# Performance work log

Measured on AMD Instinct MI355X. Metric: run time of the kernel, lower is better.

Reference implementation:

```python
import jax, jax.numpy as jnp
import numpy as np
from jax import lax

NQ = 4      # num_qubits
DEPTH = 2
DIM = 2 ** NQ  # 16

def _maxpool2(x):
    # MaxPool2d(kernel_size=2, stride=1), NCHW
    return lax.reduce_window(x, -jnp.inf, lax.max, (1, 1, 2, 2), (1, 1, 1, 1), 'VALID')

def _conv(x, w, b, stride, pad):
    y = lax.conv_general_dilated(x, w, (stride, stride), [(pad, pad), (pad, pad)],
                                 dimension_numbers=('NCHW', 'OIHW', 'NCHW'))
    return y + b[None, :, None, None]

def _apply_1q(state, gate, q):
    # state: (B, 16) complex64; gate: (2,2) shared or (B,2,2) per-sample. wire 0 = MSB.
    B = state.shape[0]
    s = state.reshape(B, 2 ** q, 2, 2 ** (NQ - 1 - q))
    sub = 'ij,bljr->blir' if gate.ndim == 2 else 'bij,bljr->blir'
    return jnp.einsum(sub, gate, s).reshape(B, DIM)

def _quantum_head(angles, weights):
    # Batched statevector simulation of: RX(angles[i]) encoding, then DEPTH x
    # [RY(w) on every wire, CZ chain], then <Z_0>, <Z_1>.
    B = angles.shape[0]
    state = jnp.zeros((B, DIM), jnp.complex64).at[:, 0].set(1.0)
    for q in range(NQ):  # RX encoding (per-sample angles)
        t = angles[:, q] * 0.5
        c = jnp.cos(t).astype(jnp.complex64)
        s = (-1j) * jnp.sin(t).astype(jnp.complex64)
        gate = jnp.stack([jnp.stack([c, s], -1), jnp.stack([s, c], -1)], -2)  # (B,2,2)
        state = _apply_1q(state, gate, q)
    idxs = jnp.arange(DIM)
    w_idx = 0
    for _ in range(DEPTH):
        for q in range(NQ):  # RY(weights) shared across batch
            t = weights[w_idx] * 0.5
            w_idx += 1
            c, s = jnp.cos(t), jnp.sin(t)
            gate = jnp.stack([jnp.stack([c, -s]), jnp.stack([s, c])]).astype(jnp.complex64)
            state = _apply_1q(state, gate, q)
        for q in range(NQ - 1):  # CZ(q, q+1): -1 phase where both bits set
            both = ((idxs >> (NQ - 1 - q)) & 1) & ((idxs >> (NQ - 2 - q)) & 1)
            phase = jnp.where(both == 1, -1.0, 1.0).astype(jnp.complex64)
            state = state * phase[None, :]
    probs = state.real ** 2 + state.imag ** 2  # (B,16) float32
    logits = []
    for q in range(2):  # expval PauliZ on wires 0,1
        sign = 1.0 - 2.0 * ((idxs >> (NQ - 1 - q)) & 1).astype(jnp.float32)
        logits.append(probs @ sign)
    return jnp.stack(logits, -1)  # (B,2)


def setup_inputs() -> dict:
    key = jax.random.key(0)
    ks = jax.random.split(key, 12)
    x = jax.random.normal(ks[0], (256, 3, 250, 250), jnp.float32)
    w1 = jax.random.normal(ks[1], (6, 3, 5, 5), jnp.float32) * 0.05
    b1 = jnp.zeros((6,), jnp.float32)
    w2 = jax.random.normal(ks[2], (15, 6, 3, 3), jnp.float32) * 0.05
    b2 = jnp.zeros((15,), jnp.float32)
    fc1_w = jax.random.normal(ks[3], (120, 55815), jnp.float32) * 0.004
    fc1_b = jnp.zeros((120,), jnp.float32)
    fc2_w = jax.random.normal(ks[4], (84, 120), jnp.float32) * 0.09
    fc2_b = jnp.zeros((84,), jnp.float32)
    fc3_w = jax.random.normal(ks[5], (4, 84), jnp.float32) * 0.1
    fc3_b = jnp.zeros((4,), jnp.float32)
    qweights = jax.random.normal(ks[6], (NQ * DEPTH,), jnp.float32)
    return {'x': x, 'w1': w1, 'b1': b1, 'w2': w2, 'b2': b2,
            'fc1_w': fc1_w, 'fc1_b': fc1_b, 'fc2_w': fc2_w, 'fc2_b': fc2_b,
            'fc3_w': fc3_w, 'fc3_b': fc3_b, 'qweights': qweights}


def reference(x, w1, b1, w2, b2, fc1_w, fc1_b, fc2_w, fc2_b, fc3_w, fc3_b, qweights):
    # Dropout layers act as identity (eval mode).
    h = jax.nn.relu(_conv(x, w1, b1, stride=2, pad=1))   # (B,6,124,124)
    h = _maxpool2(h)                                      # (B,6,123,123)
    h = jax.nn.relu(_conv(h, w2, b2, stride=2, pad=1))   # (B,15,62,62)
    h = _maxpool2(h)                                      # (B,15,61,61)
    h = h.reshape(h.shape[0], -1)                         # (B,55815)
    h = jax.nn.relu(h @ fc1_w.T + fc1_b)
    h = jax.nn.relu(h @ fc2_w.T + fc2_b)
    angles = h @ fc3_w.T + fc3_b                          # (B,4)
    logits = _quantum_head(angles, qweights)              # (B,2)
    return jax.nn.softmax(logits, axis=-1)
```

## Files before the change

kernel.cpp:

```cpp
#include <hip/hip_runtime.h>
#include <hip/hip_bf16.h>
#include <hip/hip_fp16.h>
#include <math.h>

#define B 256
#define FC1_K   55815
#define FC1_N   120
#define FC2_N   84
#define KP        57344
#define FC1_SPLIT 256
#define FC1_KC    (KP / FC1_SPLIT)

typedef __attribute__((ext_vector_type(8))) short bf16x8;
typedef __attribute__((ext_vector_type(4))) float f32x4;
typedef _Float16 half2_t __attribute__((ext_vector_type(2)));

static __device__ __forceinline__ unsigned short bf16_bits(float f) {
    __hip_bfloat16 h = __float2bfloat16(f);
    return *(unsigned short*)&h;
}
static __device__ __forceinline__ unsigned short f16_bits(float f) {
    __half h = __float2half(f);
    return *(unsigned short*)&h;
}
static __device__ __forceinline__ half2_t h2_from_u32(unsigned int u) {
    return __builtin_bit_cast(half2_t, u);
}

#define ASYNC_CP(g, l) __builtin_amdgcn_global_load_lds( \
    (const __attribute__((address_space(1))) void*)(g),  \
    (__attribute__((address_space(3))) void*)(l), 4, 0, 0)

__global__ __launch_bounds__(256) void conv1_fused_kernel(
    const float* __restrict__ x, const float* __restrict__ w1,
    const float* __restrict__ b1, const float* __restrict__ fc1_w,
    unsigned short* __restrict__ pool1, float* __restrict__ zeros,
    unsigned short* __restrict__ wb) {
    if (blockIdx.x >= 18) {
        int wid = (blockIdx.x - 18) * 256 + blockIdx.y;
        int kb = wid >> 7, n = wid & 127;
        int k0 = kb * 2048 + threadIdx.x * 8;
        bf16x8 v8;
        #pragma unroll
        for (int i = 0; i < 8; ++i) v8[i] = 0;
        if (n < FC1_N) {
            const float* src = fc1_w + (size_t)n * FC1_K + k0;
            if (k0 + 8 <= FC1_K) {
                #pragma unroll
                for (int i = 0; i < 8; ++i) v8[i] = (short)bf16_bits(src[i]);
            } else {
                #pragma unroll
                for (int i = 0; i < 8; ++i)
                    if (k0 + i < FC1_K) v8[i] = (short)bf16_bits(src[i]);
            }
        }
        *(bf16x8*)(wb + (size_t)n * KP + k0) = v8;
        return;
    }

    __shared__ __align__(16) float in_t[19 * 256 + 8];
    __shared__ __align__(16) unsigned short out_t[6 * 8 * 132];

    const int tid = threadIdx.x;
    const int wave = tid >> 6, lane = tid & 63;
    const int PB = 7 * blockIdx.x;
    const int b  = blockIdx.y;
    const int cg = tid & 31, rr = tid >> 5;
    const int iyb = 2 * PB - 1;

    if (tid < 64) zeros[tid] = 0.f;

    float acc[4][6];
    #pragma unroll
    for (int j = 0; j < 4; ++j)
        #pragma unroll
        for (int o = 0; o < 6; ++o) acc[j][o] = b1[o];

    for (int c = 0; c < 3; ++c) {
        __syncthreads();
        const float* xp = x + (size_t)(b * 3 + c) * 62500;
        #pragma unroll
        for (int i = 0; i < 19; ++i) {
            int chunk = wave * 19 + i;
            int f = chunk * 64 + lane;
            int row = f >> 8, m = f & 255;
            int iy = iyb + row, col = m - 1;
            const float* g = ((unsigned)iy < 250u && (unsigned)col < 250u)
                             ? (xp + iy * 250 + col) : zeros;
            ASYNC_CP(g, &in_t[chunk * 64]);
        }
        __syncthreads();
        #pragma unroll
        for (int ky = 0; ky < 5; ++ky) {
            const float* rp = &in_t[(2 * rr + ky) * 256 + 8 * cg];
            float f[12];
            float4 v0 = *(const float4*)rp;
            float4 v1 = *(const float4*)(rp + 4);
            float4 v2 = *(const float4*)(rp + 8);
            f[0]=v0.x; f[1]=v0.y; f[2]=v0.z; f[3]=v0.w;
            f[4]=v1.x; f[5]=v1.y; f[6]=v1.z; f[7]=v1.w;
            f[8]=v2.x; f[9]=v2.y; f[10]=v2.z; f[11]=v2.w;
            #pragma unroll
            for (int kx = 0; kx < 5; ++kx) {
                #pragma unroll
                for (int j = 0; j < 4; ++j) {
                    float xv = f[2 * j + kx];
                    #pragma unroll
                    for (int o = 0; o < 6; ++o)
                        acc[j][o] += xv * w1[(o * 3 + c) * 25 + ky * 5 + kx];
                }
            }
        }
    }
    #pragma unroll
    for (int o = 0; o < 6; ++o) {
        unsigned short h0 = f16_bits(fmaxf(acc[0][o], 0.f));
        unsigned short h1 = f16_bits(fmaxf(acc[1][o], 0.f));
        unsigned short h2 = f16_bits(fmaxf(acc[2][o], 0.f));
        unsigned short h3 = f16_bits(fmaxf(acc[3][o], 0.f));
        uint2 pk;
        pk.x = (unsigned)h0 | ((unsigned)h1 << 16);
        pk.y = (unsigned)h2 | ((unsigned)h3 << 16);
        *(uint2*)&out_t[(o * 8 + rr) * 132 + 4 * cg] = pk;
    }
    __syncthreads();
    for (int it = tid; it < 6 * 7 * 32; it += 256) {
        int g = it & 31, rem = it >> 5;
        int pyl = rem % 7, oc = rem / 7;
        int py = PB + pyl;
        if (py >= 123) continue;
        const unsigned short* q0 = &out_t[(oc * 8 + pyl) * 132 + 4 * g];
        const unsigned short* q1 = q0 + 132;
        uint2 ua = *(const uint2*)q0;
        uint2 ub = *(const uint2*)q1;
        unsigned short va[5] = {(unsigned short)(ua.x & 0xffff), (unsigned short)(ua.x >> 16),
                                (unsigned short)(ua.y & 0xffff), (unsigned short)(ua.y >> 16), q0[4]};
        unsigned short vb[5] = {(unsigned short)(ub.x & 0xffff), (unsigned short)(ub.x >> 16),
                                (unsigned short)(ub.y & 0xffff), (unsigned short)(ub.y >> 16), q1[4]};
        unsigned short* dst = pool1 + ((size_t)(b * 6 + oc) * 123 + py) * 128;
        #pragma unroll
        for (int j = 0; j < 4; ++j) {
            int px = 4 * g + j;
            if (px >= 127) continue;
            unsigned short m = 0;
            if (px <= 122) {
                unsigned short m0 = va[j] > va[j+1] ? va[j] : va[j+1];
                unsigned short m1 = vb[j] > vb[j+1] ? vb[j] : vb[j+1];
                m = m0 > m1 ? m0 : m1;
            }
            dst[1 + px] = m;
        }
        if (g == 0) dst[0] = 0;
    }
}

__global__ __launch_bounds__(128) void conv2_pool2_kernel(
    const unsigned short* __restrict__ pool1, const float* __restrict__ w2,
    const float* __restrict__ b2, unsigned short* __restrict__ A) {
    __shared__ __align__(16) unsigned int in2[17 * 64 + 8];
    __shared__ __align__(16) unsigned int wlds[540];
    __shared__ __align__(16) unsigned short out2[15 * 8 * 68];

    const int tid = threadIdx.x;
    const int wave = tid >> 6, lane = tid & 63;
    const int PB = 7 * blockIdx.x;
    const int b  = blockIdx.y;
    const int cg = tid & 15, rr = tid >> 4;
    const int iyb = 2 * PB - 1;

    for (int f = tid; f < 540; f += 128) {
        int pr = f & 1, g = f >> 1;
        int o = g % 15, r = g / 15, ky = r % 3, c = r / 3;
        const float* wsrc = w2 + (o * 6 + c) * 9 + ky * 3;
        unsigned int pk;
        if (pr == 0) pk = (unsigned)f16_bits(wsrc[0]) | ((unsigned)f16_bits(wsrc[1]) << 16);
        else         pk = (unsigned)f16_bits(wsrc[2]);
        wlds[((c * 3 + ky) * 15 + o) * 2 + pr] = pk;
    }
    if (tid < 8) in2[17 * 64 + tid] = 0;

    float acc[4][15];
    #pragma unroll
    for (int j = 0; j < 4; ++j)
        #pragma unroll
        for (int o = 0; o < 15; ++o) acc[j][o] = b2[o];

    const unsigned int* p1u = (const unsigned int*)pool1;
    for (int c = 0; c < 6; ++c) {
        __syncthreads();
        const unsigned int* pp = p1u + (size_t)(b * 6 + c) * (123 * 64);
        #pragma unroll
        for (int i = 0; i < 9; ++i) {
            int chunk = wave * 9 + i;
            if (chunk < 17) {
                int iy = iyb + chunk;
                if ((unsigned)iy < 123u) {
                    ASYNC_CP(pp + iy * 64 + lane, &in2[chunk * 64]);
                } else {
                    in2[chunk * 64 + lane] = 0;
                }
            }
        }
        __syncthreads();
        #pragma unroll
        for (int ky = 0; ky < 3; ++ky) {
            const unsigned int* rp = &in2[(2 * rr + ky) * 64 + 4 * cg];
            half2_t dd[5];
            {
                uint4 u4 = *(const uint4*)rp;
                unsigned int u5 = rp[4];
                dd[0] = h2_from_u32(u4.x); dd[1] = h2_from_u32(u4.y);
                dd[2] = h2_from_u32(u4.z); dd[3] = h2_from_u32(u4.w);
                dd[4] = h2_from_u32(u5);
            }
            const unsigned int* wrow = &wlds[(c * 3 + ky) * 30];
            unsigned int wv[30];
            #pragma unroll
            for (int i = 0; i < 30; ++i) wv[i] = wrow[i];
            #pragma unroll
            for (int j = 0; j < 4; ++j) {
                #pragma unroll
                for (int o = 0; o < 15; ++o) {
                    acc[j][o] = __builtin_amdgcn_fdot2(dd[j],     h2_from_u32(wv[o * 2]),
                                                       acc[j][o], false);
                    acc[j][o] = __builtin_amdgcn_fdot2(dd[j + 1], h2_from_u32(wv[o * 2 + 1]),
                                                       acc[j][o], false);
                }
            }
        }
    }
    #pragma unroll
    for (int o = 0; o < 15; ++o) {
        unsigned short h0 = bf16_bits(fmaxf(acc[0][o], 0.f));
        unsigned short h1 = bf16_bits(fmaxf(acc[1][o], 0.f));
        unsigned short h2 = bf16_bits(fmaxf(acc[2][o], 0.f));
        unsigned short h3 = bf16_bits(fmaxf(acc[3][o], 0.f));
        uint2 pk;
        pk.x = (unsigned)h0 | ((unsigned)h1 << 16);
        pk.y = (unsigned)h2 | ((unsigned)h3 << 16);
        *(uint2*)&out2[(o * 8 + rr) * 68 + 4 * cg] = pk;
    }
    __syncthreads();
    for (int it = tid; it < 15 * 7 * 16; it += 128) {
        int g = it & 15, rem = it >> 4;
        int pyl = rem % 7, oc = rem / 7;
        int py = PB + pyl;
        if (py >= 61) continue;
        const unsigned short* q0 = &out2[(oc * 8 + pyl) * 68 + 4 * g];
        const unsigned short* q1 = q0 + 68;
        uint2 ua = *(const uint2*)q0;
        uint2 ub = *(const uint2*)q1;
        unsigned short va[5] = {(unsigned short)(ua.x & 0xffff), (unsigned short)(ua.x >> 16),
                                (unsigned short)(ua.y & 0xffff), (unsigned short)(ua.y >> 16), q0[4]};
        unsigned short vb[5] = {(unsigned short)(ub.x & 0xffff), (unsigned short)(ub.x >> 16),
                                (unsigned short)(ub.y & 0xffff), (unsigned short)(ub.y >> 16), q1[4]};
        #pragma unroll
        for (int j = 0; j < 4; ++j) {
            int px = 4 * g + j;
            if (px < 61) {
                unsigned short m0 = va[j] > va[j+1] ? va[j] : va[j+1];
                unsigned short m1 = vb[j] > vb[j+1] ? vb[j] : vb[j+1];
                unsigned short m = m0 > m1 ? m0 : m1;
                A[(size_t)b * KP + (oc * 61 + py) * 61 + px] = m;
            }
        }
    }
}

__global__ __launch_bounds__(256) void fc1_mfma_kernel(
    const __hip_bfloat16* __restrict__ A, const __hip_bfloat16* __restrict__ W,
    float* __restrict__ partial) {
    const int wave = threadIdx.x >> 6, lane = threadIdx.x & 63;
    const int mrow = lane & 15, quad = lane >> 4;
    const int m0 = blockIdx.x * 128 + wave * 32;
    const int k0 = blockIdx.y * FC1_KC;

    f32x4 acc[2][8];
    #pragma unroll
    for (int i = 0; i < 2; ++i)
        #pragma unroll
        for (int j = 0; j < 8; ++j) acc[i][j] = (f32x4){0.f, 0.f, 0.f, 0.f};

    const short* Ap = (const short*)A;
    const short* Wp = (const short*)W;
    for (int ks = 0; ks < FC1_KC; ks += 32) {
        const int kk = k0 + ks + quad * 8;
        const bf16x8 a0 = *(const bf16x8*)(Ap + (size_t)(m0 + mrow) * KP + kk);
        const bf16x8 a1 = *(const bf16x8*)(Ap + (size_t)(m0 + 16 + mrow) * KP + kk);
        #pragma unroll
        for (int nt = 0; nt < 8; ++nt) {
            const bf16x8 bb = *(const bf16x8*)(Wp + (size_t)(nt * 16 + mrow) * KP + kk);
            acc[0][nt] = __builtin_amdgcn_mfma_f32_16x16x32_bf16(a0, bb, acc[0][nt], 0, 0, 0);
            acc[1][nt] = __builtin_amdgcn_mfma_f32_16x16x32_bf16(a1, bb, acc[1][nt], 0, 0, 0);
        }
    }
    float* po = partial + (size_t)blockIdx.y * (256 * 128);
    #pragma unroll
    for (int mt = 0; mt < 2; ++mt)
        #pragma unroll
        for (int nt = 0; nt < 8; ++nt)
            #pragma unroll
            for (int r = 0; r < 4; ++r)
                po[(m0 + mt * 16 + quad * 4 + r) * 128 + nt * 16 + mrow] = acc[mt][nt][r];
}

__global__ __launch_bounds__(512) void tail_kernel(
    const float* __restrict__ partial, const float* __restrict__ fc1_b,
    const float* __restrict__ fc2_w, const float* __restrict__ fc2_b,
    const float* __restrict__ fc3_w, const float* __restrict__ fc3_b,
    const float* __restrict__ qw, float* __restrict__ out) {
    __shared__ float h1p[4][FC1_N];
    __shared__ float h1[FC1_N];
    __shared__ float h2[FC2_N];
    __shared__ float ang[4];
    int b = blockIdx.x;
    int t = threadIdx.x;
    int grp = t >> 7, tt = t & 127;

    if (tt < FC1_N) {
        const float* p = partial + b * 128 + tt;
        float sum = 0.f;
        #pragma unroll 8
        for (int s = grp * 64; s < grp * 64 + 64; ++s) sum += p[(size_t)s * (256 * 128)];
        h1p[grp][tt] = sum;
    }
    __syncthreads();
    if (t < FC1_N)
        h1[t] = fmaxf(h1p[0][t] + h1p[1][t] + h1p[2][t] + h1p[3][t] + fc1_b[t], 0.f);
    __syncthreads();
    if (t < FC2_N) {
        float acc = fc2_b[t];
        const float* w = fc2_w + t * FC1_N;
        for (int k = 0; k < FC1_N; ++k) acc += h1[k] * w[k];
        h2[t] = fmaxf(acc, 0.f);
    }
    __syncthreads();
    if (t < 4) {
        float acc = fc3_b[t];
        const float* w = fc3_w + t * FC2_N;
        for (int k = 0; k < FC2_N; ++k) acc += h2[k] * w[k];
        ang[t] = acc;
    }
    __syncthreads();
    if (t < 16) {
        const int lane = t;
        float sr = (lane == 0) ? 1.f : 0.f, si = 0.f;
        #pragma unroll
        for (int q = 0; q < 4; ++q) {
            float th = ang[q] * 0.5f;
            float c = __cosf(th), s = __sinf(th);
            int mask = 8 >> q;
            float pr = __shfl_xor(sr, mask, 16);
            float pi = __shfl_xor(si, mask, 16);
            float nr = c * sr + s * pi;
            float ni = c * si - s * pr;
            sr = nr; si = ni;
        }
        int widx = 0;
        #pragma unroll
        for (int d = 0; d < 2; ++d) {
            #pragma unroll
            for (int q = 0; q < 4; ++q) {
                float th = qw[widx++] * 0.5f;
                float c = __cosf(th), s = __sinf(th);
                int mask = 8 >> q;
                float pr = __shfl_xor(sr, mask, 16);
                float pi = __shfl_xor(si, mask, 16);
                float sg = (lane & mask) ? s : -s;
                sr = c * sr + sg * pr;
                si = c * si + sg * pi;
            }
            #pragma unroll
            for (int q = 0; q < 3; ++q) {
                int m1 = 8 >> q, m2 = 4 >> q;
                if ((lane & m1) && (lane & m2)) { sr = -sr; si = -si; }
            }
        }
        float p = sr * sr + si * si;
        float v0 = (lane & 8) ? -p : p;
        float v1 = (lane & 4) ? -p : p;
        #pragma unroll
        for (int off = 8; off >= 1; off >>= 1) {
            v0 += __shfl_xor(v0, off, 16);
            v1 += __shfl_xor(v1, off, 16);
        }
        if (lane == 0) {
            float m = fmaxf(v0, v1);
            float e0 = expf(v0 - m), e1 = expf(v1 - m);
            float inv = 1.f / (e0 + e1);
            out[b * 2 + 0] = e0 * inv;
            out[b * 2 + 1] = e1 * inv;
        }
    }
}

extern "C" void kernel_launch(void* const* d_in, const int* in_sizes, int n_in,
                              void* d_out, int out_size, void* d_ws, size_t ws_size,
                              hipStream_t stream) {
    const float* x     = (const float*)d_in[0];
    const float* w1    = (const float*)d_in[1];
    const float* b1    = (const float*)d_in[2];
    const float* w2    = (const float*)d_in[3];
    const float* b2    = (const float*)d_in[4];
    const float* fc1_w = (const float*)d_in[5];
    const float* fc1_b = (const float*)d_in[6];
    const float* fc2_w = (const float*)d_in[7];
    const float* fc2_b = (const float*)d_in[8];
    const float* fc3_w = (const float*)d_in[9];
    const float* fc3_b = (const float*)d_in[10];
    const float* qw    = (const float*)d_in[11];
    float* out = (float*)d_out;

    char* ws = (char*)d_ws;
    const size_t O_POOL1  = 0;
    const size_t O_A      = O_POOL1 + 48365568;
    const size_t O_W      = O_A + 29360128;
    const size_t O_PART   = O_W + 14680064;
    const size_t O_ZERO   = O_PART + 33554432;
    unsigned short* pool1   = (unsigned short*)(ws + O_POOL1);
    __hip_bfloat16* A_bf16  = (__hip_bfloat16*)(ws + O_A);
    __hip_bfloat16* W_bf16  = (__hip_bfloat16*)(ws + O_W);
    float*          partial = (float*)(ws + O_PART);
    float*          zeros   = (float*)(ws + O_ZERO);

    conv1_fused_kernel<<<dim3(32, B), 256, 0, stream>>>(
        x, w1, b1, fc1_w, pool1, zeros, (unsigned short*)W_bf16);
    conv2_pool2_kernel<<<dim3(9, B), 128, 0, stream>>>(pool1, w2, b2,
                                                       (unsigned short*)A_bf16);
    fc1_mfma_kernel<<<dim3(2, FC1_SPLIT), 256, 0, stream>>>(A_bf16, W_bf16, partial);
    tail_kernel<<<B, 512, 0, stream>>>(partial, fc1_b, fc2_w, fc2_b,
                                       fc3_w, fc3_b, qw, out);
}
```

Baseline: 448.9 us.

## Split weight prep into own kernel and double-buffer conv input loads

Moves the fc1 weight bf16 conversion and the conv2 weight packing out of the conv kernels into a separate prep kernel. conv1 and conv2 now double-buffer their per-channel LDS input tiles so the async load of the next channel overlaps compute on the current one. conv1 also gets a padded LDS row stride, likely to reduce bank conflicts. conv2 reads the packed weights straight from global/constant memory instead of LDS. The cost is one extra kernel launch and more LDS per block, which may lower occupancy.

```diff
diff --git a/kernel.cpp b/kernel.cpp
--- a/kernel.cpp
+++ b/kernel.cpp
@@ -31,35 +31,50 @@
     (const __attribute__((address_space(1))) void*)(g),  \
     (__attribute__((address_space(3))) void*)(l), 4, 0, 0)
 
-__global__ __launch_bounds__(256) void conv1_fused_kernel(
+__global__ __launch_bounds__(256) void prep_kernel(
+    const float* __restrict__ fc1_w, const float* __restrict__ w2,
+    unsigned short* __restrict__ wb, unsigned int* __restrict__ w2pk,
+    float* __restrict__ zeros) {
+    const int n = blockIdx.y;
+    const int k0 = blockIdx.x * 2048 + threadIdx.x * 8;
+    bf16x8 v8;
+    #pragma unroll
+    for (int i = 0; i < 8; ++i) v8[i] = 0;
+    if (n < FC1_N) {
+        const float* src = fc1_w + (size_t)n * FC1_K + k0;
+        if (k0 + 8 <= FC1_K) {
+            #pragma unroll
+            for (int i = 0; i < 8; ++i) v8[i] = (short)bf16_bits(src[i]);
+        } else {
+            #pragma unroll
+            for (int i = 0; i < 8; ++i)
+                if (k0 + i < FC1_K) v8[i] = (short)bf16_bits(src[i]);
+        }
+    }
+    *(bf16x8*)(wb + (size_t)n * KP + k0) = v8;
+
+    if (blockIdx.x == 0 && n == 0) {
+        int t = threadIdx.x;
+        if (t < 64) zeros[t] = 0.f;
+        for (int f = t; f < 540; f += 256) {
+            int pr = f & 1, g = f >> 1;
+            int o = g % 15, r = g / 15, ky = r % 3, c = r / 3;
+            const float* wsrc = w2 + (o * 6 + c) * 9 + ky * 3;
+            unsigned int pk;
+            if (pr == 0) pk = (unsigned)f16_bits(wsrc[0]) | ((unsigned)f16_bits(wsrc[1]) << 16);
+            else         pk = (unsigned)f16_bits(wsrc[2]);
+            w2pk[((c * 3 + ky) * 15 + o) * 2 + pr] = pk;
+        }
+    }
+}
+
+#define C1_ROW 276
+__global__ __launch_bounds__(256) void conv1_pool1_kernel(
     const float* __restrict__ x, const float* __restrict__ w1,
-    const float* __restrict__ b1, const float* __restrict__ fc1_w,
-    unsigned short* __restrict__ pool1, float* __restrict__ zeros,
-    unsigned short* __restrict__ wb) {
-    if (blockIdx.x >= 18) {
-        int wid = (blockIdx.x - 18) * 256 + blockIdx.y;
-        int kb = wid >> 7, n = wid & 127;
-        int k0 = kb * 2048 + threadIdx.x * 8;
-        bf16x8 v8;
-        #pragma unroll
-        for (int i = 0; i < 8; ++i) v8[i] = 0;
-        if (n < FC1_N) {
-            const float* src = fc1_w + (size_t)n * FC1_K + k0;
-            if (k0 + 8 <= FC1_K) {
-                #pragma unroll
-                for (int i = 0; i < 8; ++i) v8[i] = (short)bf16_bits(src[i]);
-            } else {
-                #pragma unroll
-                for (int i = 0; i < 8; ++i)
-                    if (k0 + i < FC1_K) v8[i] = (short)bf16_bits(src[i]);
-            }
-        }
-        *(bf16x8*)(wb + (size_t)n * KP + k0) = v8;
-        return;
-    }
-
-    __shared__ __align__(16) float in_t[19 * 256 + 8];
-    __shared__ __align__(16) unsigned short out_t[6 * 8 * 132];
+    const float* __restrict__ b1, unsigned short* __restrict__ pool1,
+    const float* __restrict__ zeros) {
+    __shared__ __align__(16) float in_t[2][19 * C1_ROW];
+    unsigned short* out_t = (unsigned short*)&in_t[1][0];
 
     const int tid = threadIdx.x;
     const int wave = tid >> 6, lane = tid & 63;
@@ -68,7 +83,9 @@
     const int cg = tid & 31, rr = tid >> 5;
     const int iyb = 2 * PB - 1;
 
-    if (tid < 64) zeros[tid] = 0.f;
+    const int g0 = cg >> 3, o0 = 8 * (cg & 7);
+    const int a0 = g0 * 68 + o0;
+    const int a2 = (o0 < 56) ? (a0 + 8) : ((g0 + 1) * 68);
 
     float acc[4][6];
     #pragma unroll
@@ -76,27 +93,41 @@
         #pragma unroll
         for (int o = 0; o < 6; ++o) acc[j][o] = b1[o];
 
-    for (int c = 0; c < 3; ++c) {
-        __syncthreads();
-        const float* xp = x + (size_t)(b * 3 + c) * 62500;
+    {
+        const float* xp = x + (size_t)(b * 3 + 0) * 62500;
         #pragma unroll
         for (int i = 0; i < 19; ++i) {
             int chunk = wave * 19 + i;
-            int f = chunk * 64 + lane;
-            int row = f >> 8, m = f & 255;
-            int iy = iyb + row, col = m - 1;
-            const float* g = ((unsigned)iy < 250u && (unsigned)col < 250u)
-                             ? (xp + iy * 250 + col) : zeros;
-            ASYNC_CP(g, &in_t[chunk * 64]);
-        }
-        __syncthreads();
+            int row = chunk >> 2, g = chunk & 3;
+            int iy = iyb + row, col = g * 64 + lane - 1;
+            const float* gp = ((unsigned)iy < 250u && (unsigned)col < 250u)
+                              ? (xp + iy * 250 + col) : zeros;
+            ASYNC_CP(gp, &in_t[0][row * C1_ROW + g * 68]);
+        }
+    }
+    __syncthreads();
+    for (int c = 0; c < 3; ++c) {
+        if (c < 2) {
+            const float* xp = x + (size_t)(b * 3 + c + 1) * 62500;
+            float* dstb = &in_t[(c + 1) & 1][0];
+            #pragma unroll
+            for (int i = 0; i < 19; ++i) {
+                int chunk = wave * 19 + i;
+                int row = chunk >> 2, g = chunk & 3;
+                int iy = iyb + row, col = g * 64 + lane - 1;
+                const float* gp = ((unsigned)iy < 250u && (unsigned)col < 250u)
+                                  ? (xp + iy * 250 + col) : zeros;
+                ASYNC_CP(gp, dstb + row * C1_ROW + g * 68);
+            }
+        }
+        const float* bufp = &in_t[c & 1][0];
         #pragma unroll
         for (int ky = 0; ky < 5; ++ky) {
-            const float* rp = &in_t[(2 * rr + ky) * 256 + 8 * cg];
+            const float* rowp = bufp + (2 * rr + ky) * C1_ROW;
             float f[12];
-            float4 v0 = *(const float4*)rp;
-            float4 v1 = *(const float4*)(rp + 4);
-            float4 v2 = *(const float4*)(rp + 8);
+            float4 v0 = *(const float4*)(rowp + a0);
+            float4 v1 = *(const float4*)(rowp + a0 + 4);
+            float4 v2 = *(const float4*)(rowp + a2);
             f[0]=v0.x; f[1]=v0.y; f[2]=v0.z; f[3]=v0.w;
             f[4]=v1.x; f[5]=v1.y; f[6]=v1.z; f[7]=v1.w;
             f[8]=v2.x; f[9]=v2.y; f[10]=v2.z; f[11]=v2.w;
@@ -111,6 +142,7 @@
                 }
             }
         }
+        if (c < 2) __syncthreads();
     }
     #pragma unroll
     for (int o = 0; o < 6; ++o) {
@@ -155,10 +187,9 @@
 }
 
 __global__ __launch_bounds__(128) void conv2_pool2_kernel(
-    const unsigned short* __restrict__ pool1, const float* __restrict__ w2,
+    const unsigned short* __restrict__ pool1, const unsigned int* __restrict__ w2pk,
     const float* __restrict__ b2, unsigned short* __restrict__ A) {
-    __shared__ __align__(16) unsigned int in2[17 * 64 + 8];
-    __shared__ __align__(16) unsigned int wlds[540];
+    __shared__ __align__(16) unsigned int in2[2][17 * 64];
     __shared__ __align__(16) unsigned short out2[15 * 8 * 68];
 
     const int tid = threadIdx.x;
@@ -168,17 +199,6 @@
     const int cg = tid & 15, rr = tid >> 4;
     const int iyb = 2 * PB - 1;
 
-    for (int f = tid; f < 540; f += 128) {
-        int pr = f & 1, g = f >> 1;
-        int o = g % 15, r = g / 15, ky = r % 3, c = r / 3;
-        const float* wsrc = w2 + (o * 6 + c) * 9 + ky * 3;
-        unsigned int pk;
-        if (pr == 0) pk = (unsigned)f16_bits(wsrc[0]) | ((unsigned)f16_bits(wsrc[1]) << 16);
-        else         pk = (unsigned)f16_bits(wsrc[2]);
-        wlds[((c * 3 + ky) * 15 + o) * 2 + pr] = pk;
-    }
-    if (tid < 8) in2[17 * 64 + tid] = 0;
-
     float acc[4][15];
     #pragma unroll
     for (int j = 0; j < 4; ++j)
@@ -186,25 +206,38 @@
         for (int o = 0; o < 15; ++o) acc[j][o] = b2[o];
 
     const unsigned int* p1u = (const unsigned int*)pool1;
-    for (int c = 0; c < 6; ++c) {
-        __syncthreads();
-        const unsigned int* pp = p1u + (size_t)(b * 6 + c) * (123 * 64);
+
+    {
+        const unsigned int* pp = p1u + (size_t)(b * 6 + 0) * (123 * 64);
         #pragma unroll
         for (int i = 0; i < 9; ++i) {
             int chunk = wave * 9 + i;
             if (chunk < 17) {
                 int iy = iyb + chunk;
-                if ((unsigned)iy < 123u) {
-                    ASYNC_CP(pp + iy * 64 + lane, &in2[chunk * 64]);
-                } else {
-                    in2[chunk * 64 + lane] = 0;
+                if ((unsigned)iy < 123u) ASYNC_CP(pp + iy * 64 + lane, &in2[0][chunk * 64]);
+                else                     in2[0][chunk * 64 + lane] = 0;
+            }
+        }
+    }
+    __syncthreads();
+    for (int c = 0; c < 6; ++c) {
+        if (c < 5) {
+            const unsigned int* pp = p1u + (size_t)(b * 6 + c + 1) * (123 * 64);
+            unsigned int* dstb = &in2[(c + 1) & 1][0];
+            #pragma unroll
+            for (int i = 0; i < 9; ++i) {
+                int chunk = wave * 9 + i;
+                if (chunk < 17) {
+                    int iy = iyb + chunk;
+                    if ((unsigned)iy < 123u) ASYNC_CP(pp + iy * 64 + lane, dstb + chunk * 64);
+                    else                     dstb[chunk * 64 + lane] = 0;
                 }
             }
         }
-        __syncthreads();
+        const unsigned int* bufp = &in2[c & 1][0];
         #pragma unroll
         for (int ky = 0; ky < 3; ++ky) {
-            const unsigned int* rp = &in2[(2 * rr + ky) * 64 + 4 * cg];
+            const unsigned int* rp = bufp + (2 * rr + ky) * 64 + 4 * cg;
             half2_t dd[5];
             {
                 uint4 u4 = *(const uint4*)rp;
@@ -213,21 +246,19 @@
                 dd[2] = h2_from_u32(u4.z); dd[3] = h2_from_u32(u4.w);
                 dd[4] = h2_from_u32(u5);
             }
-            const unsigned int* wrow = &wlds[(c * 3 + ky) * 30];
-            unsigned int wv[30];
-            #pragma unroll
-            for (int i = 0; i < 30; ++i) wv[i] = wrow[i];
+            const unsigned int* wrow = w2pk + (c * 3 + ky) * 30;
             #pragma unroll
             for (int j = 0; j < 4; ++j) {
                 #pragma unroll
                 for (int o = 0; o < 15; ++o) {
-                    acc[j][o] = __builtin_amdgcn_fdot2(dd[j],     h2_from_u32(wv[o * 2]),
+                    acc[j][o] = __builtin_amdgcn_fdot2(dd[j],     h2_from_u32(wrow[o * 2]),
                                                        acc[j][o], false);
-                    acc[j][o] = __builtin_amdgcn_fdot2(dd[j + 1], h2_from_u32(wv[o * 2 + 1]),
+                    acc[j][o] = __builtin_amdgcn_fdot2(dd[j + 1], h2_from_u32(wrow[o * 2 + 1]),
                                                        acc[j][o], false);
                 }
             }
         }
+        if (c < 5) __syncthreads();
     }
     #pragma unroll
     for (int o = 0; o < 15; ++o) {
@@ -416,16 +447,19 @@
     const size_t O_A      = O_POOL1 + 48365568;
     const size_t O_W      = O_A + 29360128;
     const size_t O_PART   = O_W + 14680064;
-    const size_t O_ZERO   = O_PART + 33554432;
+    const size_t O_W2PK   = O_PART + 33554432;
+    const size_t O_ZERO   = O_W2PK + 4096;
     unsigned short* pool1   = (unsigned short*)(ws + O_POOL1);
     __hip_bfloat16* A_bf16  = (__hip_bfloat16*)(ws + O_A);
     __hip_bfloat16* W_bf16  = (__hip_bfloat16*)(ws + O_W);
     float*          partial = (float*)(ws + O_PART);
+    unsigned int*   w2pk    = (unsigned int*)(ws + O_W2PK);
     float*          zeros   = (float*)(ws + O_ZERO);
 
-    conv1_fused_kernel<<<dim3(32, B), 256, 0, stream>>>(
-        x, w1, b1, fc1_w, pool1, zeros, (unsigned short*)W_bf16);
-    conv2_pool2_kernel<<<dim3(9, B), 128, 0, stream>>>(pool1, w2, b2,
+    prep_kernel<<<dim3(KP / 2048, 128), 256, 0, stream>>>(
+        fc1_w, w2, (unsigned short*)W_bf16, w2pk, zeros);
+    conv1_pool1_kernel<<<dim3(18, B), 256, 0, stream>>>(x, w1, b1, pool1, zeros);
+    conv2_pool2_kernel<<<dim3(9, B), 128, 0, stream>>>(pool1, w2pk, b2,
                                                        (unsigned short*)A_bf16);
     fc1_mfma_kernel<<<dim3(2, FC1_SPLIT), 256, 0, stream>>>(A_bf16, W_bf16, partial);
     tail_kernel<<<B, 512, 0, stream>>>(partial, fc1_b, fc2_w, fc2_b,
```

Result: slower. 461.7 us (+2.9%).
